# Performance work log

Measured on AMD Instinct MI355X. Metric: run time of the kernel, lower is better.

The kernel has to match this reference:

```python
import jax, jax.numpy as jnp
import numpy as np

N_NODES = 100000
N_EDGES = 1600000
D_HID = 64  # per-party hidden width; concat of two parties -> 128


def setup_inputs() -> dict:
    key = jax.random.key(0)
    k1, k2, k3, k4, k5 = jax.random.split(key, 5)
    h1 = jax.random.normal(k1, (N_NODES, D_HID), dtype=jnp.float32)
    h2 = jax.random.normal(k2, (N_NODES, D_HID), dtype=jnp.float32)
    # Glorot-ish scale for dense layers
    W1 = jax.random.normal(k3, (2 * 2 * D_HID, 16), dtype=jnp.float32) * (1.0 / np.sqrt(2 * 2 * D_HID))
    b1 = jnp.zeros((16,), dtype=jnp.float32)
    W2 = jax.random.normal(k4, (16, 1), dtype=jnp.float32) * 0.25
    b2 = jnp.zeros((1,), dtype=jnp.float32)
    edges = jax.random.randint(k5, (2, N_EDGES), 0, N_NODES, dtype=jnp.int64)
    return {"h1": h1, "h2": h2, "W1": W1, "b1": b1, "W2": W2, "b2": b2, "edges": edges}


def reference(h1, h2, W1, b1, W2, b2, edges):
    # concat party hiddens -> node features [N, 128]
    x = jnp.concatenate([h1, h2], axis=-1)
    src, dst = edges[0], edges[1]
    # gather + concat -> edge representations [E, 256]
    edge_rep = jnp.concatenate([x[src], x[dst]], axis=-1)
    h = edge_rep @ W1 + b1          # [E, 16] (Dense(16), linear activation)
    logits = h @ W2 + b2            # [E, 1]  (Dense(1))
    return logits
```

## Files before the change

### kernel.cpp

```cpp
#include <hip/hip_runtime.h>

#define N_NODES 100000
#define N_EDGES 1600000
#define GRID_N  1250

typedef float  f32x4 __attribute__((ext_vector_type(4)));
typedef float  f32x2 __attribute__((ext_vector_type(2)));
typedef int    i32x2 __attribute__((ext_vector_type(2)));
typedef long long i64x2 __attribute__((ext_vector_type(2)));

__global__ __launch_bounds__(256) void node_kernel(
        const float* __restrict__ h1, const float* __restrict__ h2,
        const float* __restrict__ W1, const float* __restrict__ W2,
        float* __restrict__ ssrc, float* __restrict__ sdst) {
    __shared__ float wf[256];
    const int t = threadIdx.x;
    {
        float acc = 0.f;
#pragma unroll
        for (int k = 0; k < 16; ++k) acc += W1[t * 16 + k] * W2[k];
        wf[t] = acc;
    }
    __syncthreads();

    const int li = t & 15;
    const int g  = t >> 4;

    const f32x4* wf4 = (const f32x4*)wf;
    const f32x4 ws1 = wf4[li];
    const f32x4 ws2 = wf4[16 + li];
    const f32x4 wd1 = wf4[32 + li];
    const f32x4 wd2 = wf4[48 + li];

#pragma unroll
    for (int it = 0; it < 5; ++it) {
        const int node = it * (GRID_N * 16) + blockIdx.x * 16 + g;

        const f32x4 a = __builtin_nontemporal_load(
            (const f32x4*)(h1 + (size_t)node * 64) + li);
        const f32x4 b = __builtin_nontemporal_load(
            (const f32x4*)(h2 + (size_t)node * 64) + li);

        float ps = a.x * ws1.x + a.y * ws1.y + a.z * ws1.z + a.w * ws1.w
                 + b.x * ws2.x + b.y * ws2.y + b.z * ws2.z + b.w * ws2.w;
        float pd = a.x * wd1.x + a.y * wd1.y + a.z * wd1.z + a.w * wd1.w
                 + b.x * wd2.x + b.y * wd2.y + b.z * wd2.z + b.w * wd2.w;

#pragma unroll
        for (int off = 1; off < 16; off <<= 1) {
            ps += __shfl_xor(ps, off);
            pd += __shfl_xor(pd, off);
        }
        if (li == 0) { ssrc[node] = ps; sdst[node] = pd; }
    }
}

__global__ __launch_bounds__(256) void edge_kernel(
        const void* __restrict__ edges,
        const float* __restrict__ ssrc, const float* __restrict__ sdst,
        const float* __restrict__ b1, const float* __restrict__ W2,
        const float* __restrict__ b2,
        float* __restrict__ out) {
    const int t   = threadIdx.x;
    const int tid = blockIdx.x * 256 + t;

    float c = b2[0];
#pragma unroll
    for (int k = 0; k < 16; ++k) c += b1[k] * W2[k];

    const int* e32 = (const int*)edges;
    const bool is64 = (__ballot(e32[2 * (t & 63) + 1] != 0) == 0ULL);

    int s0, d0, s1, d1;
    if (is64) {
        const i64x2* es = (const i64x2*)edges;
        const i64x2* ed = es + (N_EDGES / 2);
        i64x2 se = __builtin_nontemporal_load(es + tid);
        i64x2 de = __builtin_nontemporal_load(ed + tid);
        s0 = (int)se.x; s1 = (int)se.y;
        d0 = (int)de.x; d1 = (int)de.y;
    } else {
        const i32x2* es = (const i32x2*)edges;
        const i32x2* ed = es + (N_EDGES / 2);
        i32x2 se = __builtin_nontemporal_load(es + tid);
        i32x2 de = __builtin_nontemporal_load(ed + tid);
        s0 = se.x; s1 = se.y;
        d0 = de.x; d1 = de.y;
    }

    f32x2 r;
    r.x = ssrc[s0] + sdst[d0] + c;
    r.y = ssrc[s1] + sdst[d1] + c;
    __builtin_nontemporal_store(r, (f32x2*)out + tid);
}

extern "C" void kernel_launch(void* const* d_in, const int* in_sizes, int n_in,
                              void* d_out, int out_size, void* d_ws, size_t ws_size,
                              hipStream_t stream) {
    const float* h1 = (const float*)d_in[0];
    const float* h2 = (const float*)d_in[1];
    const float* W1 = (const float*)d_in[2];
    const float* b1 = (const float*)d_in[3];
    const float* W2 = (const float*)d_in[4];
    const float* b2 = (const float*)d_in[5];
    const void*  edges = d_in[6];

    float* ssrc = (float*)d_ws;
    float* sdst = ssrc + N_NODES;
    float* out  = (float*)d_out;

    node_kernel<<<GRID_N, 256, 0, stream>>>(h1, h2, W1, W2, ssrc, sdst);
    edge_kernel<<<N_EDGES / 512, 256, 0, stream>>>(edges, ssrc, sdst, b1, W2, b2, out);
}
```

Measured before the change: 31.29 us.

## Pack per-node src/dst scores as half2 and process four edges per thread

```diff
diff --git a/kernel.cpp b/kernel.cpp
--- a/kernel.cpp
+++ b/kernel.cpp
@@ -1,18 +1,19 @@
 #include <hip/hip_runtime.h>
+#include <hip/hip_fp16.h>
 
 #define N_NODES 100000
 #define N_EDGES 1600000
-#define GRID_N  1250
+#define GRID_N  2048
+#define NBI     6250
 
 typedef float  f32x4 __attribute__((ext_vector_type(4)));
-typedef float  f32x2 __attribute__((ext_vector_type(2)));
-typedef int    i32x2 __attribute__((ext_vector_type(2)));
+typedef int    i32x4 __attribute__((ext_vector_type(4)));
 typedef long long i64x2 __attribute__((ext_vector_type(2)));
 
 __global__ __launch_bounds__(256) void node_kernel(
         const float* __restrict__ h1, const float* __restrict__ h2,
         const float* __restrict__ W1, const float* __restrict__ W2,
-        float* __restrict__ ssrc, float* __restrict__ sdst) {
+        __half2* __restrict__ pair) {
     __shared__ float wf[256];
     const int t = threadIdx.x;
     {
@@ -32,9 +33,8 @@
     const f32x4 wd1 = wf4[32 + li];
     const f32x4 wd2 = wf4[48 + li];
 
-#pragma unroll
-    for (int it = 0; it < 5; ++it) {
-        const int node = it * (GRID_N * 16) + blockIdx.x * 16 + g;
+    for (int bi = blockIdx.x; bi < NBI; bi += GRID_N) {
+        const int node = bi * 16 + g;
 
         const f32x4 a = __builtin_nontemporal_load(
             (const f32x4*)(h1 + (size_t)node * 64) + li);
@@ -51,13 +51,13 @@
             ps += __shfl_xor(ps, off);
             pd += __shfl_xor(pd, off);
         }
-        if (li == 0) { ssrc[node] = ps; sdst[node] = pd; }
+        if (li == 0) pair[node] = __floats2half2_rn(ps, pd);
     }
 }
 
 __global__ __launch_bounds__(256) void edge_kernel(
         const void* __restrict__ edges,
-        const float* __restrict__ ssrc, const float* __restrict__ sdst,
+        const __half2* __restrict__ pair,
         const float* __restrict__ b1, const float* __restrict__ W2,
         const float* __restrict__ b2,
         float* __restrict__ out) {
@@ -71,27 +71,37 @@
     const int* e32 = (const int*)edges;
     const bool is64 = (__ballot(e32[2 * (t & 63) + 1] != 0) == 0ULL);
 
-    int s0, d0, s1, d1;
+    if (tid >= N_EDGES / 4) return;
+
+    int s[4], d[4];
     if (is64) {
         const i64x2* es = (const i64x2*)edges;
         const i64x2* ed = es + (N_EDGES / 2);
-        i64x2 se = __builtin_nontemporal_load(es + tid);
-        i64x2 de = __builtin_nontemporal_load(ed + tid);
-        s0 = (int)se.x; s1 = (int)se.y;
-        d0 = (int)de.x; d1 = (int)de.y;
+        i64x2 s01 = __builtin_nontemporal_load(es + 2 * tid);
+        i64x2 s23 = __builtin_nontemporal_load(es + 2 * tid + 1);
+        i64x2 d01 = __builtin_nontemporal_load(ed + 2 * tid);
+        i64x2 d23 = __builtin_nontemporal_load(ed + 2 * tid + 1);
+        s[0] = (int)s01.x; s[1] = (int)s01.y; s[2] = (int)s23.x; s[3] = (int)s23.y;
+        d[0] = (int)d01.x; d[1] = (int)d01.y; d[2] = (int)d23.x; d[3] = (int)d23.y;
     } else {
-        const i32x2* es = (const i32x2*)edges;
-        const i32x2* ed = es + (N_EDGES / 2);
-        i32x2 se = __builtin_nontemporal_load(es + tid);
-        i32x2 de = __builtin_nontemporal_load(ed + tid);
-        s0 = se.x; s1 = se.y;
-        d0 = de.x; d1 = de.y;
+        const i32x4* es = (const i32x4*)edges;
+        const i32x4* ed = (const i32x4*)((const int*)edges + N_EDGES);
+        i32x4 sv = __builtin_nontemporal_load(es + tid);
+        i32x4 dv = __builtin_nontemporal_load(ed + tid);
+        s[0] = sv.x; s[1] = sv.y; s[2] = sv.z; s[3] = sv.w;
+        d[0] = dv.x; d[1] = dv.y; d[2] = dv.z; d[3] = dv.w;
     }
 
-    f32x2 r;
-    r.x = ssrc[s0] + sdst[d0] + c;
-    r.y = ssrc[s1] + sdst[d1] + c;
-    __builtin_nontemporal_store(r, (f32x2*)out + tid);
+    __half2 ph[4], qh[4];
+#pragma unroll
+    for (int i = 0; i < 4; ++i) { ph[i] = pair[s[i]]; qh[i] = pair[d[i]]; }
+
+    f32x4 r;
+    r.x = __low2float(ph[0]) + __high2float(qh[0]) + c;
+    r.y = __low2float(ph[1]) + __high2float(qh[1]) + c;
+    r.z = __low2float(ph[2]) + __high2float(qh[2]) + c;
+    r.w = __low2float(ph[3]) + __high2float(qh[3]) + c;
+    __builtin_nontemporal_store(r, (f32x4*)out + tid);
 }
 
 extern "C" void kernel_launch(void* const* d_in, const int* in_sizes, int n_in,
@@ -105,10 +115,9 @@
     const float* b2 = (const float*)d_in[5];
     const void*  edges = d_in[6];
 
-    float* ssrc = (float*)d_ws;
-    float* sdst = ssrc + N_NODES;
-    float* out  = (float*)d_out;
+    __half2* pair = (__half2*)d_ws;
+    float*   out  = (float*)d_out;
 
-    node_kernel<<<GRID_N, 256, 0, stream>>>(h1, h2, W1, W2, ssrc, sdst);
-    edge_kernel<<<N_EDGES / 512, 256, 0, stream>>>(edges, ssrc, sdst, b1, W2, b2, out);
+    node_kernel<<<GRID_N, 256, 0, stream>>>(h1, h2, W1, W2, pair);
+    edge_kernel<<<(N_EDGES / 4 + 255) / 256, 256, 0, stream>>>(edges, pair, b1, W2, b2, out);
 }
```

Result: slower. 32.04 us (+2.4%).
